# Performance work log

Measured on AMD Instinct MI355X. Metric: run time of the kernel, lower is better.

The kernel has to match this reference:

```python
import jax, jax.numpy as jnp
import numpy as np

E, K, D = 50000, 8, 256
NH = 4
HD = D // NH
SCALE = HD ** -0.5
EPS = 1e-8


def setup_inputs() -> dict:
    key = jax.random.key(0)
    ks = jax.random.split(key, 16)
    p = lambda k, shp: (jax.random.normal(k, shp, dtype=jnp.float32) * 0.02)
    return {
        "x_i": jax.random.normal(ks[0], (E, D), dtype=jnp.float32),
        "x_j": jax.random.normal(ks[1], (E, D), dtype=jnp.float32),
        "h_seq_i": jax.random.normal(ks[2], (E, K, D), dtype=jnp.float32),
        "h_seq_j": jax.random.normal(ks[3], (E, K, D), dtype=jnp.float32),
        "edge_emb": jax.random.normal(ks[4], (E, D), dtype=jnp.float32),
        "Wq": p(ks[5], (D, D)), "bq": jnp.zeros((D,), jnp.float32),
        "Wk": p(ks[6], (D, D)), "bk": jnp.zeros((D,), jnp.float32),
        "We1": p(ks[7], (D, D // 2)), "be1": jnp.zeros((D // 2,), jnp.float32),
        "We2": p(ks[8], (D // 2, 1)), "be2": jnp.zeros((1,), jnp.float32),
        "Wo1": p(ks[9], (3, 16)), "bo1": jnp.zeros((16,), jnp.float32),
        "Wo2": p(ks[10], (16, 1)), "bo2": jnp.zeros((1,), jnp.float32),
    }


def reference(x_i, x_j, h_seq_i, h_seq_j, edge_emb,
              Wq, bq, Wk, bk, We1, be1, We2, be2, Wo1, bo1, Wo2, bo2):
    # (A) attribute alignment: cosine similarity mapped to (0,1)
    num = jnp.sum(x_i * x_j, axis=-1)
    den = jnp.maximum(jnp.linalg.norm(x_i, axis=-1), EPS) * \
          jnp.maximum(jnp.linalg.norm(x_j, axis=-1), EPS)
    attr_score = (num / den + 1.0) / 2.0  # [E]

    # (B) activity alignment: tiny cross-attention, mean of softmax diagonal
    Q = (jnp.einsum('ekd,df->ekf', h_seq_i, Wq) + bq).reshape(E, K, NH, HD)
    Kv = (jnp.einsum('ekd,df->ekf', h_seq_j, Wk) + bk).reshape(E, K, NH, HD)
    scores = jnp.einsum('eqhd,ekhd->ehqk', Q, Kv) * SCALE  # [E,NH,K,K]
    attn = jax.nn.softmax(scores, axis=-1)
    diag = jnp.diagonal(attn, axis1=-2, axis2=-1)  # [E,NH,K]
    activity_score = diag.mean(axis=(-1, -2))  # [E]

    # (C) edge plausibility MLP (exact GELU as in torch default)
    h = jax.nn.gelu(edge_emb @ We1 + be1, approximate=False)
    edge_score = jax.nn.sigmoid((h @ We2 + be2)[..., 0])  # [E]

    signals = jnp.stack([attr_score, activity_score, edge_score], axis=-1)  # [E,3]
    out = jax.nn.gelu(signals @ Wo1 + bo1, approximate=False) @ Wo2 + bo2
    return jax.nn.sigmoid(out[..., 0])  # [E]
```

## Files before the change

kernel.cpp:

```cpp
#include <hip/hip_runtime.h>

#define E_TOT   50000
#define DD      256
#define KSEQ    8
#define NHEAD   4
#define HDIM    64
#define TE      4
#define SCALE_V 0.125f

typedef __attribute__((ext_vector_type(4))) float f32x4;
typedef __attribute__((ext_vector_type(8))) short short8;

__device__ __forceinline__ unsigned short f2bf(float f) {
    unsigned u = __float_as_uint(f);
    u += 0x7fffu + ((u >> 16) & 1u);
    return (unsigned short)(u >> 16);
}
__device__ __forceinline__ float bf2f(unsigned short h) {
    return __uint_as_float(((unsigned)h) << 16);
}
__device__ __forceinline__ float gelu_exact(float x) {
    return 0.5f * x * (1.0f + erff(x * 0.70710678118654752440f));
}
__device__ __forceinline__ float sigmoidf(float x) {
    return 1.0f / (1.0f + __expf(-x));
}

__global__ void prep_weights(const float* __restrict__ Wq,
                             const float* __restrict__ Wk,
                             const float* __restrict__ We1,
                             unsigned short* __restrict__ wqT,
                             unsigned short* __restrict__ wkT,
                             unsigned short* __restrict__ wb1) {
    int i = blockIdx.x * 256 + threadIdx.x;
    if (i < 131072) {
        int which = i >> 16;
        int j = i & 65535;
        int k = j >> 8, n = j & 255;
        const float* W = which ? Wk : Wq;
        unsigned short* o = which ? wkT : wqT;
        o[n * 256 + k] = f2bf(W[j]);
    } else {
        int j = i - 131072;
        wb1[j] = f2bf(We1[j]);
    }
}

__global__ void score_attr_edge(const float* __restrict__ x_i,
                                const float* __restrict__ x_j,
                                const float* __restrict__ emb,
                                const unsigned short* __restrict__ wb1,
                                const float* __restrict__ be1,
                                const float* __restrict__ We2,
                                const float* __restrict__ be2,
                                float* __restrict__ attr_out,
                                float* __restrict__ edge_out) {
    __shared__ float sEmb[4][DD];
    const int wv = threadIdx.x >> 6;
    const int l  = threadIdx.x & 63;
    const int e  = blockIdx.x * 4 + wv;

    f32x4 a = *(const f32x4*)(x_i + (size_t)e * DD + l * 4);
    f32x4 b = *(const f32x4*)(x_j + (size_t)e * DD + l * 4);
    f32x4 ev = *(const f32x4*)(emb + (size_t)e * DD + l * 4);
    float dot = a[0]*b[0] + a[1]*b[1] + a[2]*b[2] + a[3]*b[3];
    float ni  = a[0]*a[0] + a[1]*a[1] + a[2]*a[2] + a[3]*a[3];
    float nj  = b[0]*b[0] + b[1]*b[1] + b[2]*b[2] + b[3]*b[3];
    #pragma unroll
    for (int off = 1; off < 64; off <<= 1) {
        dot += __shfl_xor(dot, off);
        ni  += __shfl_xor(ni,  off);
        nj  += __shfl_xor(nj,  off);
    }
    float na = fmaxf(sqrtf(ni), 1e-8f);
    float nb = fmaxf(sqrtf(nj), 1e-8f);
    if (l == 0) attr_out[e] = (dot / (na * nb) + 1.0f) * 0.5f;

    sEmb[wv][l*4+0] = ev[0]; sEmb[wv][l*4+1] = ev[1];
    sEmb[wv][l*4+2] = ev[2]; sEmb[wv][l*4+3] = ev[3];
    __syncthreads();

    float acc0 = 0.f, acc1 = 0.f;
    #pragma unroll 8
    for (int k = 0; k < DD; ++k) {
        float ek = sEmb[wv][k];
        unsigned u = *(const unsigned*)(wb1 + k * 128 + 2 * l);
        acc0 = fmaf(ek, bf2f((unsigned short)(u & 0xffffu)), acc0);
        acc1 = fmaf(ek, bf2f((unsigned short)(u >> 16)),     acc1);
    }
    float h0 = gelu_exact(acc0 + be1[2 * l]);
    float h1 = gelu_exact(acc1 + be1[2 * l + 1]);
    float s  = h0 * We2[2 * l] + h1 * We2[2 * l + 1];
    #pragma unroll
    for (int off = 1; off < 64; off <<= 1) s += __shfl_xor(s, off);
    if (l == 0) edge_out[e] = sigmoidf(s + be2[0]);
}

__device__ __forceinline__ void do_gemm(const unsigned short (*A)[DD + 8],
                                        const unsigned short* __restrict__ Wt,
                                        f32x4 acc[2][4], int l, int w) {
    const int lr = l & 15, lq = l >> 4;
    #pragma unroll
    for (int ks = 0; ks < 8; ++ks) {
        const short8 a0 = *(const short8*)&A[lr][ks * 32 + lq * 8];
        const short8 a1 = *(const short8*)&A[16 + lr][ks * 32 + lq * 8];
        #pragma unroll
        for (int n = 0; n < 4; ++n) {
            const int col = (w * 4 + n) * 16 + lr;
            const short8 bv = *(const short8*)(Wt + col * 256 + ks * 32 + lq * 8);
            acc[0][n] = __builtin_amdgcn_mfma_f32_16x16x32_bf16(a0, bv, acc[0][n], 0, 0, 0);
            acc[1][n] = __builtin_amdgcn_mfma_f32_16x16x32_bf16(a1, bv, acc[1][n], 0, 0, 0);
        }
    }
}

__device__ __forceinline__ void writeback(unsigned short (*A)[DD + 8],
                                          const f32x4 acc[2][4],
                                          const float* __restrict__ bias,
                                          int l, int w) {
    const int lr = l & 15, lq = l >> 4;
    #pragma unroll
    for (int n = 0; n < 4; ++n) {
        const int col = (w * 4 + n) * 16 + lr;
        const float bs = bias[col];
        #pragma unroll
        for (int m = 0; m < 2; ++m) {
            #pragma unroll
            for (int v = 0; v < 4; ++v) {
                const int row = m * 16 + lq * 4 + v;
                A[row][col] = f2bf(acc[m][n][v] + bs);
            }
        }
    }
}

__global__ __launch_bounds__(256, 4)
void fused_attn(const float* __restrict__ h_i,
                const float* __restrict__ h_j,
                const unsigned short* __restrict__ wqT,
                const unsigned short* __restrict__ wkT,
                const float* __restrict__ bq,
                const float* __restrict__ bk,
                const float* __restrict__ Wo1,
                const float* __restrict__ bo1,
                const float* __restrict__ Wo2,
                const float* __restrict__ bo2,
                const float* __restrict__ attr_ws,
                const float* __restrict__ edge_ws,
                float* __restrict__ out) {
    __shared__ unsigned short Abf[2][TE * KSEQ][DD + 8];
    __shared__ float actLds[TE];

    const int t = threadIdx.x;
    const int w = t >> 6;
    const int l = t & 63;
    const size_t base = (size_t)blockIdx.x * (TE * KSEQ * DD);

    f32x4 stg[16];
    #pragma unroll
    for (int i = 0; i < 16; ++i) {
        const int f  = i * 256 + t;
        const float* src = (f >> 11) ? h_j : h_i;
        stg[i] = *(const f32x4*)(src + base + (size_t)(f & 2047) * 4);
    }
    #pragma unroll
    for (int i = 0; i < 16; ++i) {
        const int f  = i * 256 + t;
        const int T  = f >> 11;
        const int ff = f & 2047;
        ushort4 u = make_ushort4(f2bf(stg[i][0]), f2bf(stg[i][1]),
                                 f2bf(stg[i][2]), f2bf(stg[i][3]));
        *(ushort4*)&Abf[T][ff >> 6][(ff & 63) * 4] = u;
    }
    __syncthreads();

    {
        f32x4 acc[2][4] = {};
        do_gemm(Abf[0], wqT, acc, l, w);
        __syncthreads();
        writeback(Abf[0], acc, bq, l, w);
    }
    {
        f32x4 acc[2][4] = {};
        do_gemm(Abf[1], wkT, acc, l, w);
        __syncthreads();
        writeback(Abf[1], acc, bk, l, w);
    }
    __syncthreads();

    if (t < 128) {
        const int e = t >> 5, h = (t >> 3) & 3, q = t & 7;
        float qv[64];
        #pragma unroll
        for (int c = 0; c < 8; ++c) {
            short8 v = *(const short8*)&Abf[0][e * 8 + q][h * 64 + c * 8];
            #pragma unroll
            for (int j = 0; j < 8; ++j) qv[c * 8 + j] = bf2f((unsigned short)v[j]);
        }
        float sc[8];
        #pragma unroll
        for (int k = 0; k < 8; ++k) {
            float d = 0.f;
            #pragma unroll
            for (int c = 0; c < 8; ++c) {
                short8 kv = *(const short8*)&Abf[1][e * 8 + k][h * 64 + c * 8];
                #pragma unroll
                for (int j = 0; j < 8; ++j) d = fmaf(qv[c * 8 + j], bf2f((unsigned short)kv[j]), d);
            }
            sc[k] = d * SCALE_V;
        }
        float mx = sc[0];
        #pragma unroll
        for (int k = 1; k < 8; ++k) mx = fmaxf(mx, sc[k]);
        float sum = 0.f, pd = 0.f;
        #pragma unroll
        for (int k = 0; k < 8; ++k) {
            float p = __expf(sc[k] - mx);
            sum += p;
            if (k == q) pd = p;
        }
        float dg = pd / sum;
        #pragma unroll
        for (int off = 1; off < 32; off <<= 1) dg += __shfl_xor(dg, off);
        if ((t & 31) == 0) actLds[e] = dg * (1.0f / 32.0f);
    }
    __syncthreads();

    if (t < TE) {
        const int ge = blockIdx.x * TE + t;
        const float s0 = attr_ws[ge];
        const float s1 = actLds[t];
        const float s2 = edge_ws[ge];
        float acc = bo2[0];
        #pragma unroll
        for (int j = 0; j < 16; ++j) {
            float z = s0 * Wo1[j] + s1 * Wo1[16 + j] + s2 * Wo1[32 + j] + bo1[j];
            acc += gelu_exact(z) * Wo2[j];
        }
        out[ge] = sigmoidf(acc);
    }
}

extern "C" void kernel_launch(void* const* d_in, const int* in_sizes, int n_in,
                              void* d_out, int out_size, void* d_ws, size_t ws_size,
                              hipStream_t stream) {
    const float* x_i  = (const float*)d_in[0];
    const float* x_j  = (const float*)d_in[1];
    const float* h_i  = (const float*)d_in[2];
    const float* h_j  = (const float*)d_in[3];
    const float* emb  = (const float*)d_in[4];
    const float* Wq   = (const float*)d_in[5];
    const float* bq   = (const float*)d_in[6];
    const float* Wk   = (const float*)d_in[7];
    const float* bk   = (const float*)d_in[8];
    const float* We1  = (const float*)d_in[9];
    const float* be1  = (const float*)d_in[10];
    const float* We2  = (const float*)d_in[11];
    const float* be2  = (const float*)d_in[12];
    const float* Wo1  = (const float*)d_in[13];
    const float* bo1  = (const float*)d_in[14];
    const float* Wo2  = (const float*)d_in[15];
    const float* bo2  = (const float*)d_in[16];
    float* out = (float*)d_out;

    unsigned short* wqT = (unsigned short*)d_ws;
    unsigned short* wkT = wqT + 65536;
    unsigned short* wb1 = wkT + 65536;
    float* attr_ws = (float*)((char*)d_ws + 327680);
    float* edge_ws = attr_ws + E_TOT;

    prep_weights<<<640, 256, 0, stream>>>(Wq, Wk, We1, wqT, wkT, wb1);
    score_attr_edge<<<E_TOT / 4, 256, 0, stream>>>(x_i, x_j, emb, wb1, be1, We2, be2,
                                                   attr_ws, edge_ws);
    fused_attn<<<E_TOT / TE, 256, 0, stream>>>(h_i, h_j, wqT, wkT, bq, bk,
                                               Wo1, bo1, Wo2, bo2,
                                               attr_ws, edge_ws, out);
}
```

Before: 569.8 us.

## Make fused attention kernel persistent with register-prefetched next tile

Converts fused_attn into a persistent kernel with a fixed 512-block grid that loops over edge groups. The next group's h_i/h_j fp32 loads are issued into registers before the Q and K MFMA GEMMs, so memory latency overlaps with compute. Both GEMMs are now merged so they run back to back with a single barrier. Occupancy hints drop to 2 blocks per SIMD unit because of the extra live registers, and the fixed grid may underfill the GPU and reduce latency hiding from other waves.

```diff
diff --git a/kernel.cpp b/kernel.cpp
--- a/kernel.cpp
+++ b/kernel.cpp
@@ -6,7 +6,9 @@
 #define NHEAD   4
 #define HDIM    64
 #define TE      4
+#define NGROUP  (E_TOT / TE)
 #define SCALE_V 0.125f
+#define PGRID   512
 
 typedef __attribute__((ext_vector_type(4))) float f32x4;
 typedef __attribute__((ext_vector_type(8))) short short8;
@@ -96,6 +98,19 @@
     if (l == 0) edge_out[e] = sigmoidf(s + be2[0]);
 }
 
+__device__ __forceinline__ void issue_loads(f32x4 stg[16],
+                                            const float* __restrict__ h_i,
+                                            const float* __restrict__ h_j,
+                                            int g, int t) {
+    const size_t base = (size_t)g * (TE * KSEQ * DD);
+    #pragma unroll
+    for (int i = 0; i < 16; ++i) {
+        const int f = i * 256 + t;
+        const float* src = (f >> 11) ? h_j : h_i;
+        stg[i] = *(const f32x4*)(src + base + (size_t)(f & 2047) * 4);
+    }
+}
+
 __device__ __forceinline__ void do_gemm(const unsigned short (*A)[DD + 8],
                                         const unsigned short* __restrict__ Wt,
                                         f32x4 acc[2][4], int l, int w) {
@@ -134,7 +149,7 @@
     }
 }
 
-__global__ __launch_bounds__(256, 4)
+__global__ __launch_bounds__(256, 2)
 void fused_attn(const float* __restrict__ h_i,
                 const float* __restrict__ h_j,
                 const unsigned short* __restrict__ wqT,
@@ -154,90 +169,90 @@
     const int t = threadIdx.x;
     const int w = t >> 6;
     const int l = t & 63;
-    const size_t base = (size_t)blockIdx.x * (TE * KSEQ * DD);
+    const int nwg = gridDim.x;
 
     f32x4 stg[16];
-    #pragma unroll
-    for (int i = 0; i < 16; ++i) {
-        const int f  = i * 256 + t;
-        const float* src = (f >> 11) ? h_j : h_i;
-        stg[i] = *(const f32x4*)(src + base + (size_t)(f & 2047) * 4);
-    }
-    #pragma unroll
-    for (int i = 0; i < 16; ++i) {
-        const int f  = i * 256 + t;
-        const int T  = f >> 11;
-        const int ff = f & 2047;
-        ushort4 u = make_ushort4(f2bf(stg[i][0]), f2bf(stg[i][1]),
-                                 f2bf(stg[i][2]), f2bf(stg[i][3]));
-        *(ushort4*)&Abf[T][ff >> 6][(ff & 63) * 4] = u;
-    }
-    __syncthreads();
-
-    {
-        f32x4 acc[2][4] = {};
-        do_gemm(Abf[0], wqT, acc, l, w);
-        __syncthreads();
-        writeback(Abf[0], acc, bq, l, w);
-    }
-    {
-        f32x4 acc[2][4] = {};
-        do_gemm(Abf[1], wkT, acc, l, w);
-        __syncthreads();
-        writeback(Abf[1], acc, bk, l, w);
-    }
-    __syncthreads();
-
-    if (t < 128) {
-        const int e = t >> 5, h = (t >> 3) & 3, q = t & 7;
-        float qv[64];
+    int g = blockIdx.x;
+    if (g < NGROUP) issue_loads(stg, h_i, h_j, g, t);
+
+    for (; g < NGROUP; g += nwg) {
+        __syncthreads();
+
         #pragma unroll
-        for (int c = 0; c < 8; ++c) {
-            short8 v = *(const short8*)&Abf[0][e * 8 + q][h * 64 + c * 8];
-            #pragma unroll
-            for (int j = 0; j < 8; ++j) qv[c * 8 + j] = bf2f((unsigned short)v[j]);
-        }
-        float sc[8];
-        #pragma unroll
-        for (int k = 0; k < 8; ++k) {
-            float d = 0.f;
+        for (int i = 0; i < 16; ++i) {
+            const int f  = i * 256 + t;
+            const int T  = f >> 11;
+            const int ff = f & 2047;
+            ushort4 u = make_ushort4(f2bf(stg[i][0]), f2bf(stg[i][1]),
+                                     f2bf(stg[i][2]), f2bf(stg[i][3]));
+            *(ushort4*)&Abf[T][ff >> 6][(ff & 63) * 4] = u;
+        }
+        __syncthreads();
+
+        if (g + nwg < NGROUP) issue_loads(stg, h_i, h_j, g + nwg, t);
+        __builtin_amdgcn_sched_barrier(0);
+
+        f32x4 accQ[2][4] = {};
+        f32x4 accK[2][4] = {};
+        do_gemm(Abf[0], wqT, accQ, l, w);
+        do_gemm(Abf[1], wkT, accK, l, w);
+        __syncthreads();
+        writeback(Abf[0], accQ, bq, l, w);
+        writeback(Abf[1], accK, bk, l, w);
+        __syncthreads();
+
+        if (t < 128) {
+            const int e = t >> 5, h = (t >> 3) & 3, q = t & 7;
+            float qv[64];
             #pragma unroll
             for (int c = 0; c < 8; ++c) {
-                short8 kv = *(const short8*)&Abf[1][e * 8 + k][h * 64 + c * 8];
+                short8 v = *(const short8*)&Abf[0][e * 8 + q][h * 64 + c * 8];
                 #pragma unroll
-                for (int j = 0; j < 8; ++j) d = fmaf(qv[c * 8 + j], bf2f((unsigned short)kv[j]), d);
-            }
-            sc[k] = d * SCALE_V;
-        }
-        float mx = sc[0];
-        #pragma unroll
-        for (int k = 1; k < 8; ++k) mx = fmaxf(mx, sc[k]);
-        float sum = 0.f, pd = 0.f;
-        #pragma unroll
-        for (int k = 0; k < 8; ++k) {
-            float p = __expf(sc[k] - mx);
-            sum += p;
-            if (k == q) pd = p;
-        }
-        float dg = pd / sum;
-        #pragma unroll
-        for (int off = 1; off < 32; off <<= 1) dg += __shfl_xor(dg, off);
-        if ((t & 31) == 0) actLds[e] = dg * (1.0f / 32.0f);
-    }
-    __syncthreads();
-
-    if (t < TE) {
-        const int ge = blockIdx.x * TE + t;
-        const float s0 = attr_ws[ge];
-        const float s1 = actLds[t];
-        const float s2 = edge_ws[ge];
-        float acc = bo2[0];
-        #pragma unroll
-        for (int j = 0; j < 16; ++j) {
-            float z = s0 * Wo1[j] + s1 * Wo1[16 + j] + s2 * Wo1[32 + j] + bo1[j];
-            acc += gelu_exact(z) * Wo2[j];
-        }
-        out[ge] = sigmoidf(acc);
+                for (int j = 0; j < 8; ++j) qv[c * 8 + j] = bf2f((unsigned short)v[j]);
+            }
+            float sc[8];
+            #pragma unroll
+            for (int k = 0; k < 8; ++k) {
+                float d = 0.f;
+                #pragma unroll
+                for (int c = 0; c < 8; ++c) {
+                    short8 kv = *(const short8*)&Abf[1][e * 8 + k][h * 64 + c * 8];
+                    #pragma unroll
+                    for (int j = 0; j < 8; ++j)
+                        d = fmaf(qv[c * 8 + j], bf2f((unsigned short)kv[j]), d);
+                }
+                sc[k] = d * SCALE_V;
+            }
+            float mx = sc[0];
+            #pragma unroll
+            for (int k = 1; k < 8; ++k) mx = fmaxf(mx, sc[k]);
+            float sum = 0.f, pd = 0.f;
+            #pragma unroll
+            for (int k = 0; k < 8; ++k) {
+                float p = __expf(sc[k] - mx);
+                sum += p;
+                if (k == q) pd = p;
+            }
+            float dg = pd / sum;
+            #pragma unroll
+            for (int off = 1; off < 32; off <<= 1) dg += __shfl_xor(dg, off);
+            if ((t & 31) == 0) actLds[e] = dg * (1.0f / 32.0f);
+        }
+        __syncthreads();
+
+        if (t < TE) {
+            const int ge = g * TE + t;
+            const float s0 = attr_ws[ge];
+            const float s1 = actLds[t];
+            const float s2 = edge_ws[ge];
+            float acc = bo2[0];
+            #pragma unroll
+            for (int j = 0; j < 16; ++j) {
+                float z = s0 * Wo1[j] + s1 * Wo1[16 + j] + s2 * Wo1[32 + j] + bo1[j];
+                acc += gelu_exact(z) * Wo2[j];
+            }
+            out[ge] = sigmoidf(acc);
+        }
     }
 }
 
@@ -272,7 +287,7 @@
     prep_weights<<<640, 256, 0, stream>>>(Wq, Wk, We1, wqT, wkT, wb1);
     score_attr_edge<<<E_TOT / 4, 256, 0, stream>>>(x_i, x_j, emb, wb1, be1, We2, be2,
                                                    attr_ws, edge_ws);
-    fused_attn<<<E_TOT / TE, 256, 0, stream>>>(h_i, h_j, wqT, wkT, bq, bk,
-                                               Wo1, bo1, Wo2, bo2,
-                                               attr_ws, edge_ws, out);
-}
+    fused_attn<<<PGRID, 256, 0, stream>>>(h_i, h_j, wqT, wkT, bq, bk,
+                                          Wo1, bo1, Wo2, bo2,
+                                          attr_ws, edge_ws, out);
+}
```

Measured after the change: 681.4 us. +19.6%, slower.
